# Optimization experiments

Measured on AMD Instinct MI355X. Metric: run time of the kernel, lower is better.

## Reference

```python
import jax, jax.numpy as jnp
import numpy as np

B, T, IN = 32, 1024, 256
H = 128          # hidden_size
NL = 2           # num_layers
NC = 4           # num_classes
F2 = 2 * H       # bidirectional feature size


def _lstm_dir(xs, w_ih, w_hh, b_ih, b_hh, reverse):
    # xs: [T, B, in]; w_ih: [4H, in]; w_hh: [4H, H]
    if reverse:
        xs = xs[::-1]
    h0 = jnp.zeros((xs.shape[1], H), xs.dtype)
    c0 = jnp.zeros((xs.shape[1], H), xs.dtype)

    def step(carry, xt):
        h, c = carry
        g = xt @ w_ih.T + b_ih + h @ w_hh.T + b_hh  # [B, 4H]
        i, f, gg, o = jnp.split(g, 4, axis=-1)       # PyTorch gate order i,f,g,o
        c = jax.nn.sigmoid(f) * c + jax.nn.sigmoid(i) * jnp.tanh(gg)
        h = jax.nn.sigmoid(o) * jnp.tanh(c)
        return (h, c), h

    _, hs = jax.lax.scan(step, (h0, c0), xs)  # [T, B, H]
    if reverse:
        hs = hs[::-1]
    return hs


def setup_inputs() -> dict:
    key = jax.random.key(0)
    ks = jax.random.split(key, 12)
    s = 0.05
    x = jax.random.normal(ks[0], (B, T, IN), jnp.float32)
    # stacked LSTM params: [layer, direction, ...]; layer0 in = IN, layer1 in = 2H = IN
    w_ih = jax.random.normal(ks[1], (NL, 2, 4 * H, IN), jnp.float32) * s
    w_hh = jax.random.normal(ks[2], (NL, 2, 4 * H, H), jnp.float32) * s
    b_ih = jax.random.normal(ks[3], (NL, 2, 4 * H), jnp.float32) * s
    b_hh = jax.random.normal(ks[4], (NL, 2, 4 * H), jnp.float32) * s
    wq = jax.random.normal(ks[5], (F2, F2), jnp.float32) * s
    wk = jax.random.normal(ks[6], (F2, F2), jnp.float32) * s
    wv = jax.random.normal(ks[7], (F2, F2), jnp.float32) * s
    bq = jax.random.normal(ks[8], (F2,), jnp.float32) * s
    bk = jax.random.normal(ks[9], (F2,), jnp.float32) * s
    bv = jax.random.normal(ks[10], (F2,), jnp.float32) * s
    w_fc = jax.random.normal(ks[11], (NC, F2), jnp.float32) * s
    b_fc = jnp.zeros((NC,), jnp.float32)
    return {"x": x, "w_ih": w_ih, "w_hh": w_hh, "b_ih": b_ih, "b_hh": b_hh,
            "wq": wq, "wk": wk, "wv": wv, "bq": bq, "bk": bk, "bv": bv,
            "w_fc": w_fc, "b_fc": b_fc}


def reference(x, w_ih, w_hh, b_ih, b_hh, wq, wk, wv, bq, bk, bv, w_fc, b_fc):
    # --- biLSTM (eval mode: inter-layer dropout inactive) ---
    xs = jnp.swapaxes(x, 0, 1)  # time-major [T, B, IN]
    for l in range(NL):
        fwd = _lstm_dir(xs, w_ih[l, 0], w_hh[l, 0], b_ih[l, 0], b_hh[l, 0], False)
        bwd = _lstm_dir(xs, w_ih[l, 1], w_hh[l, 1], b_ih[l, 1], b_hh[l, 1], True)
        xs = jnp.concatenate([fwd, bwd], axis=-1)  # [T, B, 2H]
    out = jnp.swapaxes(xs, 0, 1)  # [B, T, 2H]
    # --- naive full self-attention ---
    q = out @ wq.T + bq
    k = out @ wk.T + bk
    v = out @ wv.T + bv
    scores = jnp.einsum('btd,bsd->bts', q, k) / jnp.sqrt(jnp.float32(F2))
    attn = jax.nn.softmax(scores, axis=-1)          # [B, T, T]
    ctx = jnp.einsum('bts,bsd->btd', attn, v)       # [B, T, 2H]
    # --- FC head on last timestep ---
    return ctx[:, -1, :] @ w_fc.T + b_fc            # [B, NC]
```

## Files before the change

### kernel.cpp

```cpp
#include <hip/hip_runtime.h>
#include <math.h>
#include <stdint.h>

#define BB 32
#define TT 1024
#define HH 128
#define G4 512
#define CH 16
#define XPS 516

typedef _Float16 half2_t __attribute__((ext_vector_type(2)));
typedef _Float16 half8_t __attribute__((ext_vector_type(8)));
typedef float f32x4 __attribute__((ext_vector_type(4)));

__device__ __forceinline__ float fdot2f(half2_t a, half2_t b, float c) {
    return __builtin_amdgcn_fdot2(a, b, c, false);
}
__device__ __forceinline__ float rcpf(float x) {
    return __builtin_amdgcn_rcpf(x);
}
__device__ __forceinline__ float dpp_xor1(float x) {
    return __builtin_bit_cast(float, __builtin_amdgcn_update_dpp(
        0, __builtin_bit_cast(int, x), 0xB1, 0xF, 0xF, true));
}
__device__ __forceinline__ float dpp_xor2(float x) {
    return __builtin_bit_cast(float, __builtin_amdgcn_update_dpp(
        0, __builtin_bit_cast(int, x), 0x4E, 0xF, 0xF, true));
}
__device__ __forceinline__ void bar_lgkm() {
    asm volatile("s_waitcnt lgkmcnt(0)\n\ts_barrier" ::: "memory");
}

__global__ __launch_bounds__(256) void cvt_wih(
    const float* __restrict__ w, _Float16* __restrict__ o)
{
    const int i = (blockIdx.x * 256 + threadIdx.x) * 4;
    float4 f = *(const float4*)(w + i);
    half2_t t[2] = { half2_t{(_Float16)f.x, (_Float16)f.y},
                     half2_t{(_Float16)f.z, (_Float16)f.w} };
    *(float2*)(o + i) = *(float2*)t;
}

__global__ __launch_bounds__(512, 1) void lstm_fused(
    const float* __restrict__ x_in,
    const _Float16* __restrict__ wih16_l,
    const float* __restrict__ b_ih_l,
    const float* __restrict__ b_hh_l,
    const float* __restrict__ w_hh_l,
    float* __restrict__ out)
{
    const int b = blockIdx.x & 31;
    const int d = blockIdx.x >> 5;
    const int tid = threadIdx.x;
    const int wvid = tid >> 6;
    const int l = tid & 63;
    const int s = l & 3;
    const int g = l >> 2;
    const int j = (wvid << 4) | g;

    __shared__ __align__(16) _Float16 hs[HH];
    __shared__ __align__(16) float xp[2][CH * XPS];
    __shared__ __align__(16) half2_t xr[2][CH * 128];
    __shared__ __align__(16) float obuf[CH * HH];

    half2_t wv[4][16];
#pragma unroll
    for (int G = 0; G < 4; ++G) {
        const float* wr = w_hh_l + (size_t)(d * G4 + 128 * G + j) * HH + 32 * s;
#pragma unroll
        for (int q4 = 0; q4 < 8; ++q4) {
            float4 f = *(const float4*)(wr + 4 * q4);
            wv[G][2 * q4]     = half2_t{(_Float16)f.x, (_Float16)f.y};
            wv[G][2 * q4 + 1] = half2_t{(_Float16)f.z, (_Float16)f.w};
        }
    }

    const int acol0 = wvid * 64 + (l & 15);
    const _Float16* wn = wih16_l + ((size_t)d * G4 + acol0) * 256 + (l >> 4) * 8;
    const float bias0 = b_ih_l[d * G4 + acol0]      + b_hh_l[d * G4 + acol0];
    const float bias1 = b_ih_l[d * G4 + acol0 + 16] + b_hh_l[d * G4 + acol0 + 16];
    const float bias2 = b_ih_l[d * G4 + acol0 + 32] + b_hh_l[d * G4 + acol0 + 32];
    const float bias3 = b_ih_l[d * G4 + acol0 + 48] + b_hh_l[d * G4 + acol0 + 48];

    const int cbase = ((acol0 & 127) << 2) + (acol0 >> 7);

    const float* xbase = x_in + (size_t)b * TT * 256;

    const int a_noswz = (l & 15) * 512 + (l >> 4) * 16;
    const int a_swz   = (l & 7) << 4;
    const int w_swz_byte = (tid * 16) ^ (((tid >> 5) & 7) << 4);

#pragma unroll 1
    for (int p = 0; p < 2; ++p) {
        const int tlo = d ? (1008 - p * CH) : p * CH;
        const float* gs = xbase + (size_t)tlo * 256 + tid * 8;
        float4 f0 = *(const float4*)gs;
        float4 f1 = *(const float4*)(gs + 4);
        half2_t t4[4] = { half2_t{(_Float16)f0.x, (_Float16)f0.y},
                          half2_t{(_Float16)f0.z, (_Float16)f0.w},
                          half2_t{(_Float16)f1.x, (_Float16)f1.y},
                          half2_t{(_Float16)f1.z, (_Float16)f1.w} };
        *(float4*)((char*)xr[p] + w_swz_byte) = *(float4*)t4;
    }
    __syncthreads();

    f32x4 acc0 = {bias0, bias0, bias0, bias0};
    f32x4 acc1 = {bias1, bias1, bias1, bias1};
    f32x4 acc2 = {bias2, bias2, bias2, bias2};
    f32x4 acc3 = {bias3, bias3, bias3, bias3};

#pragma unroll
    for (int kt = 0; kt < 8; ++kt) {
        half8_t af = *(const half8_t*)((const char*)xr[0] + ((a_noswz + kt * 64) ^ a_swz));
        acc0 = __builtin_amdgcn_mfma_f32_16x16x32_f16(af, *(const half8_t*)(wn +         kt * 32), acc0, 0, 0, 0);
        acc1 = __builtin_amdgcn_mfma_f32_16x16x32_f16(af, *(const half8_t*)(wn +  4096 + kt * 32), acc1, 0, 0, 0);
        acc2 = __builtin_amdgcn_mfma_f32_16x16x32_f16(af, *(const half8_t*)(wn +  8192 + kt * 32), acc2, 0, 0, 0);
        acc3 = __builtin_amdgcn_mfma_f32_16x16x32_f16(af, *(const half8_t*)(wn + 12288 + kt * 32), acc3, 0, 0, 0);
    }
    {
        const int rb = (l >> 4) * 4;
#pragma unroll
        for (int q = 0; q < 4; ++q) {
            const int ix = (rb + q) * XPS + cbase;
            xp[0][ix]       = acc0[q];
            xp[0][ix + 64]  = acc1[q];
            xp[0][ix + 128] = acc2[q];
            xp[0][ix + 192] = acc3[q];
        }
    }
    acc0 = (f32x4){bias0, bias0, bias0, bias0};
    acc1 = (f32x4){bias1, bias1, bias1, bias1};
    acc2 = (f32x4){bias2, bias2, bias2, bias2};
    acc3 = (f32x4){bias3, bias3, bias3, bias3};

    if (tid < 64) ((half2_t*)hs)[tid] = half2_t{(_Float16)0.f, (_Float16)0.f};
    float c = 0.f;
    float* ob = out + (size_t)b * TT * 256 + d * HH;
    __syncthreads();

    float4 rg0 = {}, rg1 = {};
    for (int ck = 0; ck < 64; ++ck) {
        const int cur = ck & 1;
        const bool doproj = (ck + 1 < 64);
        if (ck + 2 < 64) {
            const int tlo2 = d ? (1008 - (ck + 2) * CH) : (ck + 2) * CH;
            const float* gs = xbase + (size_t)tlo2 * 256 + tid * 8;
            rg0 = *(const float4*)gs;
            rg1 = *(const float4*)(gs + 4);
        }
        const float* xb = xp[cur];
        const char* xr_rd = (const char*)xr[cur ^ 1];

        auto rec_step = [&](int si) {
            const int lds_t = d ? (CH - 1 - si) : si;
            const float4 xg4 = *(const float4*)&xb[lds_t * XPS + (j << 2)];

            const float4* hp = (const float4*)(hs + 32 * s);
            float4 hA = hp[0], hB = hp[1], hC = hp[2], hD = hp[3];
            half2_t hh[16];
            hh[0]  = __builtin_bit_cast(half2_t, hA.x);
            hh[1]  = __builtin_bit_cast(half2_t, hA.y);
            hh[2]  = __builtin_bit_cast(half2_t, hA.z);
            hh[3]  = __builtin_bit_cast(half2_t, hA.w);
            hh[4]  = __builtin_bit_cast(half2_t, hB.x);
            hh[5]  = __builtin_bit_cast(half2_t, hB.y);
            hh[6]  = __builtin_bit_cast(half2_t, hB.z);
            hh[7]  = __builtin_bit_cast(half2_t, hB.w);
            hh[8]  = __builtin_bit_cast(half2_t, hC.x);
            hh[9]  = __builtin_bit_cast(half2_t, hC.y);
            hh[10] = __builtin_bit_cast(half2_t, hC.z);
            hh[11] = __builtin_bit_cast(half2_t, hC.w);
            hh[12] = __builtin_bit_cast(half2_t, hD.x);
            hh[13] = __builtin_bit_cast(half2_t, hD.y);
            hh[14] = __builtin_bit_cast(half2_t, hD.z);
            hh[15] = __builtin_bit_cast(half2_t, hD.w);

            float a0 = 0.f, a1 = 0.f, a2 = 0.f, a3 = 0.f;
            float e0 = 0.f, e1 = 0.f, e2 = 0.f, e3 = 0.f;
#pragma unroll
            for (int kk = 0; kk < 8; ++kk) {
                a0 = fdot2f(wv[0][kk], hh[kk], a0);
                a1 = fdot2f(wv[1][kk], hh[kk], a1);
                a2 = fdot2f(wv[2][kk], hh[kk], a2);
                a3 = fdot2f(wv[3][kk], hh[kk], a3);
                e0 = fdot2f(wv[0][kk + 8], hh[kk + 8], e0);
                e1 = fdot2f(wv[1][kk + 8], hh[kk + 8], e1);
                e2 = fdot2f(wv[2][kk + 8], hh[kk + 8], e2);
                e3 = fdot2f(wv[3][kk + 8], hh[kk + 8], e3);
            }
            a0 += e0; a1 += e1; a2 += e2; a3 += e3;

            a0 += dpp_xor1(a0); a0 += dpp_xor2(a0);
            a1 += dpp_xor1(a1); a1 += dpp_xor2(a1);
            a2 += dpp_xor1(a2); a2 += dpp_xor2(a2);
            a3 += dpp_xor1(a3); a3 += dpp_xor2(a3);

            const float gi = rcpf(1.f + __expf(-(a0 + xg4.x)));
            const float gf = rcpf(1.f + __expf(-(a1 + xg4.y)));
            const float gg = 1.f - 2.f * rcpf(1.f + __expf(2.f * (a2 + xg4.z)));
            const float go = rcpf(1.f + __expf(-(a3 + xg4.w)));
            c = gf * c + gi * gg;
            const float th = 1.f - 2.f * rcpf(1.f + __expf(2.f * c));
            const float h = go * th;
            if (s == 0) {
                hs[j] = (_Float16)h;
                obuf[si * HH + j] = h;
            }
        };

        half8_t gbEA = {}, gbEB = {}, gbOA = {}, gbOB = {};
        if (doproj) {
            gbEA = *(const half8_t*)(wn);
            gbEB = *(const half8_t*)(wn + 4096);
        }

#pragma unroll 1
        for (int sp = 0; sp < CH / 2; ++sp) {
            const int kt = sp;
            half8_t afrag = {};
            if (doproj) {
                afrag = *(const half8_t*)(xr_rd + ((a_noswz + kt * 64) ^ a_swz));
                gbOA = *(const half8_t*)(wn +  8192 + kt * 32);
                gbOB = *(const half8_t*)(wn + 12288 + kt * 32);
            }
            rec_step(2 * sp);
            if (doproj) {
                acc0 = __builtin_amdgcn_mfma_f32_16x16x32_f16(afrag, gbEA, acc0, 0, 0, 0);
                acc1 = __builtin_amdgcn_mfma_f32_16x16x32_f16(afrag, gbEB, acc1, 0, 0, 0);
            }
            bar_lgkm();
            if (doproj) {
                const int ktn = (kt + 1) & 7;
                gbEA = *(const half8_t*)(wn +        ktn * 32);
                gbEB = *(const half8_t*)(wn + 4096 + ktn * 32);
            }
            rec_step(2 * sp + 1);
            if (doproj) {
                acc2 = __builtin_amdgcn_mfma_f32_16x16x32_f16(afrag, gbOA, acc2, 0, 0, 0);
                acc3 = __builtin_amdgcn_mfma_f32_16x16x32_f16(afrag, gbOB, acc3, 0, 0, 0);
            }
            bar_lgkm();
        }

        {
            const int idx = tid * 4;
            const int sf = idx >> 7, jf = idx & 127;
            const int sg = ck * CH + sf;
            const int t  = d ? (TT - 1 - sg) : sg;
            float4 o0 = *(const float4*)&obuf[idx];
            *(float4*)&ob[(size_t)t * 256 + jf] = o0;
        }
        if (doproj) {
            float* xpn = xp[cur ^ 1];
            const int rb = (l >> 4) * 4;
#pragma unroll
            for (int q = 0; q < 4; ++q) {
                const int ix = (rb + q) * XPS + cbase;
                xpn[ix]       = acc0[q];
                xpn[ix + 64]  = acc1[q];
                xpn[ix + 128] = acc2[q];
                xpn[ix + 192] = acc3[q];
            }
            acc0 = (f32x4){bias0, bias0, bias0, bias0};
            acc1 = (f32x4){bias1, bias1, bias1, bias1};
            acc2 = (f32x4){bias2, bias2, bias2, bias2};
            acc3 = (f32x4){bias3, bias3, bias3, bias3};
        }
        if (ck + 2 < 64) {
            half2_t t4[4] = { half2_t{(_Float16)rg0.x, (_Float16)rg0.y},
                              half2_t{(_Float16)rg0.z, (_Float16)rg0.w},
                              half2_t{(_Float16)rg1.x, (_Float16)rg1.y},
                              half2_t{(_Float16)rg1.z, (_Float16)rg1.w} };
            *(float4*)((char*)xr[cur] + w_swz_byte) = *(float4*)t4;
        }
        __syncthreads();
    }
}

__global__ __launch_bounds__(1024) void attn_kernel(
    const float* __restrict__ out1,
    const float* __restrict__ wq, const float* __restrict__ bq,
    const float* __restrict__ wk,
    const float* __restrict__ wv, const float* __restrict__ bv,
    const float* __restrict__ wfc, const float* __restrict__ bfc,
    float* __restrict__ outp)
{
    const int b = blockIdx.x;
    const int tid = threadIdx.x;
    const int n = tid & 255, qq = tid >> 8;

    __shared__ float xl[256], q[256], u[256], cx[256];
    __shared__ __align__(16) float r[256];
    __shared__ float sc[TT];
    __shared__ float red[1024];
    __shared__ float part[4][256];

    const float* ob = out1 + (size_t)b * TT * 256;

    if (tid < 256) xl[tid] = ob[(size_t)(TT - 1) * 256 + tid];
    __syncthreads();

    {
        float a = 0.f;
        const float* wr = wq + (size_t)n * 256 + qq * 64;
        const float* xq = xl + qq * 64;
#pragma unroll 8
        for (int k = 0; k < 64; ++k) a += xq[k] * wr[k];
        part[qq][n] = a;
    }
    __syncthreads();
    if (tid < 256) q[tid] = bq[tid] + part[0][tid] + part[1][tid] + part[2][tid] + part[3][tid];
    __syncthreads();

    {
        float a = 0.f;
        const float* wkp = wk + (size_t)(qq * 64) * 256 + n;
#pragma unroll 8
        for (int dd = 0; dd < 64; ++dd) a += q[qq * 64 + dd] * wkp[(size_t)dd * 256];
        part[qq][n] = a;
    }
    __syncthreads();
    if (tid < 256) r[tid] = part[0][tid] + part[1][tid] + part[2][tid] + part[3][tid];
    __syncthreads();

    {
        const int wave = tid >> 6, lane = tid & 63;
        float4 r4 = *(const float4*)&r[lane * 4];
        for (int t = wave; t < TT; t += 16) {
            float4 o4 = *(const float4*)(ob + (size_t)t * 256 + lane * 4);
            float p = r4.x * o4.x + r4.y * o4.y + r4.z * o4.z + r4.w * o4.w;
#pragma unroll
            for (int off = 32; off > 0; off >>= 1) p += __shfl_down(p, off, 64);
            if (lane == 0) sc[t] = p * 0.0625f;
        }
    }
    __syncthreads();

    float v = sc[tid];
    red[tid] = v; __syncthreads();
    for (int st = 512; st > 0; st >>= 1) {
        if (tid < st) red[tid] = fmaxf(red[tid], red[tid + st]);
        __syncthreads();
    }
    const float mx = red[0]; __syncthreads();
    const float e = expf(v - mx);
    sc[tid] = e;
    red[tid] = e; __syncthreads();
    for (int st = 512; st > 0; st >>= 1) {
        if (tid < st) red[tid] += red[tid + st];
        __syncthreads();
    }
    const float inv = 1.f / red[0];
    __syncthreads();

    {
        float a = 0.f;
        const float* op = ob + (size_t)(qq * 256) * 256 + n;
        const float* sp = sc + qq * 256;
#pragma unroll 4
        for (int t = 0; t < 256; ++t) a += sp[t] * op[(size_t)t * 256];
        part[qq][n] = a;
    }
    __syncthreads();
    if (tid < 256) u[tid] = (part[0][tid] + part[1][tid] + part[2][tid] + part[3][tid]) * inv;
    __syncthreads();

    {
        float a = 0.f;
        const float* wr = wv + (size_t)n * 256 + qq * 64;
#pragma unroll 8
        for (int k = 0; k < 64; ++k) a += u[qq * 64 + k] * wr[k];
        part[qq][n] = a;
    }
    __syncthreads();
    if (tid < 256) cx[tid] = bv[tid] + part[0][tid] + part[1][tid] + part[2][tid] + part[3][tid];
    __syncthreads();

    if (tid < 4) {
        float o = bfc[tid];
        for (int k = 0; k < 256; ++k) o += cx[k] * wfc[tid * 256 + k];
        outp[b * 4 + tid] = o;
    }
}

extern "C" void kernel_launch(void* const* d_in, const int* in_sizes, int n_in,
                              void* d_out, int out_size, void* d_ws, size_t ws_size,
                              hipStream_t stream)
{
    const float* x    = (const float*)d_in[0];
    const float* w_ih = (const float*)d_in[1];
    const float* w_hh = (const float*)d_in[2];
    const float* b_ih = (const float*)d_in[3];
    const float* b_hh = (const float*)d_in[4];
    const float* wq   = (const float*)d_in[5];
    const float* wk   = (const float*)d_in[6];
    const float* wv   = (const float*)d_in[7];
    const float* bq   = (const float*)d_in[8];
    const float* bv   = (const float*)d_in[10];
    const float* wfc  = (const float*)d_in[11];
    const float* bfcv = (const float*)d_in[12];
    float* outp = (float*)d_out;

    float* ws = (float*)d_ws;
    _Float16* wih16 = (_Float16*)ws;
    float* out0 = ws + 262144;
    float* out1 = out0 + 8388608;

    cvt_wih<<<512, 256, 0, stream>>>(w_ih, wih16);

    lstm_fused<<<64, 512, 0, stream>>>(x, wih16, b_ih, b_hh, w_hh, out0);
    lstm_fused<<<64, 512, 0, stream>>>(out0, wih16 + 262144, b_ih + 1024, b_hh + 1024,
                                       w_hh + 2 * 512 * 128, out1);
    attn_kernel<<<32, 1024, 0, stream>>>(out1, wq, bq, wk, wv, bv, wfc, bfcv, outp);
}
```

Before: 1.688 ms.

## Keep input-projection weights in registers and stage x prefetch via global_load_lds

Preloads all W_ih fp16 fragments for the input projection into registers once, instead of reloading them from global memory on every chunk. The next chunk of x is now copied by async global-to-LDS loads into a staging buffer, then converted to fp16 after a vmcnt wait, rather than held in registers across the chunk. The inner step loop is fully unrolled. This adds heavy register pressure (128 extra VGPRs on top of the W_hh fragments), which risks spills or lower occupancy. The staged data is read by different threads than the ones that loaded it, and only a per-thread vmcnt wait guards that read.

```diff
diff --git a/kernel.cpp b/kernel.cpp
--- a/kernel.cpp
+++ b/kernel.cpp
@@ -12,6 +12,8 @@
 typedef _Float16 half2_t __attribute__((ext_vector_type(2)));
 typedef _Float16 half8_t __attribute__((ext_vector_type(8)));
 typedef float f32x4 __attribute__((ext_vector_type(4)));
+typedef __attribute__((address_space(3))) uint32_t lds_u32;
+typedef __attribute__((address_space(1))) const uint32_t glb_u32;
 
 __device__ __forceinline__ float fdot2f(half2_t a, half2_t b, float c) {
     return __builtin_amdgcn_fdot2(a, b, c, false);
@@ -62,6 +64,7 @@
     __shared__ __align__(16) float xp[2][CH * XPS];
     __shared__ __align__(16) half2_t xr[2][CH * 128];
     __shared__ __align__(16) float obuf[CH * HH];
+    __shared__ __align__(16) float xstage[CH * 256];
 
     half2_t wv[4][16];
 #pragma unroll
@@ -81,6 +84,15 @@
     const float bias1 = b_ih_l[d * G4 + acol0 + 16] + b_hh_l[d * G4 + acol0 + 16];
     const float bias2 = b_ih_l[d * G4 + acol0 + 32] + b_hh_l[d * G4 + acol0 + 32];
     const float bias3 = b_ih_l[d * G4 + acol0 + 48] + b_hh_l[d * G4 + acol0 + 48];
+
+    half8_t wf0[8], wf1[8], wf2[8], wf3[8];
+#pragma unroll
+    for (int kt = 0; kt < 8; ++kt) {
+        wf0[kt] = *(const half8_t*)(wn +         kt * 32);
+        wf1[kt] = *(const half8_t*)(wn +  4096 + kt * 32);
+        wf2[kt] = *(const half8_t*)(wn +  8192 + kt * 32);
+        wf3[kt] = *(const half8_t*)(wn + 12288 + kt * 32);
+    }
 
     const int cbase = ((acol0 & 127) << 2) + (acol0 >> 7);
 
@@ -112,10 +124,10 @@
 #pragma unroll
     for (int kt = 0; kt < 8; ++kt) {
         half8_t af = *(const half8_t*)((const char*)xr[0] + ((a_noswz + kt * 64) ^ a_swz));
-        acc0 = __builtin_amdgcn_mfma_f32_16x16x32_f16(af, *(const half8_t*)(wn +         kt * 32), acc0, 0, 0, 0);
-        acc1 = __builtin_amdgcn_mfma_f32_16x16x32_f16(af, *(const half8_t*)(wn +  4096 + kt * 32), acc1, 0, 0, 0);
-        acc2 = __builtin_amdgcn_mfma_f32_16x16x32_f16(af, *(const half8_t*)(wn +  8192 + kt * 32), acc2, 0, 0, 0);
-        acc3 = __builtin_amdgcn_mfma_f32_16x16x32_f16(af, *(const half8_t*)(wn + 12288 + kt * 32), acc3, 0, 0, 0);
+        acc0 = __builtin_amdgcn_mfma_f32_16x16x32_f16(af, wf0[kt], acc0, 0, 0, 0);
+        acc1 = __builtin_amdgcn_mfma_f32_16x16x32_f16(af, wf1[kt], acc1, 0, 0, 0);
+        acc2 = __builtin_amdgcn_mfma_f32_16x16x32_f16(af, wf2[kt], acc2, 0, 0, 0);
+        acc3 = __builtin_amdgcn_mfma_f32_16x16x32_f16(af, wf3[kt], acc3, 0, 0, 0);
     }
     {
         const int rb = (l >> 4) * 4;
@@ -138,15 +150,18 @@
     float* ob = out + (size_t)b * TT * 256 + d * HH;
     __syncthreads();
 
-    float4 rg0 = {}, rg1 = {};
     for (int ck = 0; ck < 64; ++ck) {
         const int cur = ck & 1;
         const bool doproj = (ck + 1 < 64);
         if (ck + 2 < 64) {
             const int tlo2 = d ? (1008 - (ck + 2) * CH) : (ck + 2) * CH;
-            const float* gs = xbase + (size_t)tlo2 * 256 + tid * 8;
-            rg0 = *(const float4*)gs;
-            rg1 = *(const float4*)(gs + 4);
+            const float* gsrc = xbase + (size_t)tlo2 * 256;
+#pragma unroll
+            for (int cc = 0; cc < 2; ++cc)
+                __builtin_amdgcn_global_load_lds(
+                    (glb_u32*)(gsrc + tid * 4 + cc * 2048),
+                    (lds_u32*)&xstage[tid * 4 + cc * 2048],
+                    16, 0, 0);
         }
         const float* xb = xp[cur];
         const char* xr_rd = (const char*)xr[cur ^ 1];
@@ -208,36 +223,21 @@
             }
         };
 
-        half8_t gbEA = {}, gbEB = {}, gbOA = {}, gbOB = {};
-        if (doproj) {
-            gbEA = *(const half8_t*)(wn);
-            gbEB = *(const half8_t*)(wn + 4096);
-        }
-
-#pragma unroll 1
+#pragma unroll
         for (int sp = 0; sp < CH / 2; ++sp) {
-            const int kt = sp;
             half8_t afrag = {};
-            if (doproj) {
-                afrag = *(const half8_t*)(xr_rd + ((a_noswz + kt * 64) ^ a_swz));
-                gbOA = *(const half8_t*)(wn +  8192 + kt * 32);
-                gbOB = *(const half8_t*)(wn + 12288 + kt * 32);
-            }
+            if (doproj)
+                afrag = *(const half8_t*)(xr_rd + ((a_noswz + sp * 64) ^ a_swz));
             rec_step(2 * sp);
             if (doproj) {
-                acc0 = __builtin_amdgcn_mfma_f32_16x16x32_f16(afrag, gbEA, acc0, 0, 0, 0);
-                acc1 = __builtin_amdgcn_mfma_f32_16x16x32_f16(afrag, gbEB, acc1, 0, 0, 0);
+                acc0 = __builtin_amdgcn_mfma_f32_16x16x32_f16(afrag, wf0[sp], acc0, 0, 0, 0);
+                acc1 = __builtin_amdgcn_mfma_f32_16x16x32_f16(afrag, wf1[sp], acc1, 0, 0, 0);
             }
             bar_lgkm();
-            if (doproj) {
-                const int ktn = (kt + 1) & 7;
-                gbEA = *(const half8_t*)(wn +        ktn * 32);
-                gbEB = *(const half8_t*)(wn + 4096 + ktn * 32);
-            }
             rec_step(2 * sp + 1);
             if (doproj) {
-                acc2 = __builtin_amdgcn_mfma_f32_16x16x32_f16(afrag, gbOA, acc2, 0, 0, 0);
-                acc3 = __builtin_amdgcn_mfma_f32_16x16x32_f16(afrag, gbOB, acc3, 0, 0, 0);
+                acc2 = __builtin_amdgcn_mfma_f32_16x16x32_f16(afrag, wf2[sp], acc2, 0, 0, 0);
+                acc3 = __builtin_amdgcn_mfma_f32_16x16x32_f16(afrag, wf3[sp], acc3, 0, 0, 0);
             }
             bar_lgkm();
         }
@@ -267,10 +267,13 @@
             acc3 = (f32x4){bias3, bias3, bias3, bias3};
         }
         if (ck + 2 < 64) {
-            half2_t t4[4] = { half2_t{(_Float16)rg0.x, (_Float16)rg0.y},
-                              half2_t{(_Float16)rg0.z, (_Float16)rg0.w},
-                              half2_t{(_Float16)rg1.x, (_Float16)rg1.y},
-                              half2_t{(_Float16)rg1.z, (_Float16)rg1.w} };
+            asm volatile("s_waitcnt vmcnt(0)" ::: "memory");
+            float4 f0 = *(const float4*)&xstage[tid * 8];
+            float4 f1 = *(const float4*)&xstage[tid * 8 + 4];
+            half2_t t4[4] = { half2_t{(_Float16)f0.x, (_Float16)f0.y},
+                              half2_t{(_Float16)f0.z, (_Float16)f0.w},
+                              half2_t{(_Float16)f1.x, (_Float16)f1.y},
+                              half2_t{(_Float16)f1.z, (_Float16)f1.w} };
             *(float4*)((char*)xr[cur] + w_swz_byte) = *(float4*)t4;
         }
         __syncthreads();
```

Result: slower. 1.767 ms (+4.7%).

## Split attention head into three kernels spreading time chunks across more blocks

Applied to the files above, without the earlier changes.

Replaces the single 32-block attention kernel with three kernels: one that computes the query-key projection vector per batch, one with 256 blocks that each score 128 timesteps and accumulate an unnormalised context and softmax denominator through global atomics, and a final kernel that normalises, applies the value projection and the FC head. This spreads the bandwidth-heavy pass over out1 across many more CUs. The max subtraction is dropped from the softmax, which risks overflow for large scores, and float atomics make summation order nondeterministic. Two extra launches are added.

```diff
diff --git a/kernel.cpp b/kernel.cpp
--- a/kernel.cpp
+++ b/kernel.cpp
@@ -277,103 +277,93 @@
     }
 }
 
-__global__ __launch_bounds__(1024) void attn_kernel(
-    const float* __restrict__ out1,
-    const float* __restrict__ wq, const float* __restrict__ bq,
-    const float* __restrict__ wk,
-    const float* __restrict__ wv, const float* __restrict__ bv,
-    const float* __restrict__ wfc, const float* __restrict__ bfc,
-    float* __restrict__ outp)
+
+__global__ __launch_bounds__(256) void attn_qr(
+    const float* __restrict__ out1, const float* __restrict__ wq,
+    const float* __restrict__ bq,   const float* __restrict__ wk,
+    float* __restrict__ r_ws, float* __restrict__ ctxw, float* __restrict__ den)
 {
     const int b = blockIdx.x;
     const int tid = threadIdx.x;
-    const int n = tid & 255, qq = tid >> 8;
-
-    __shared__ float xl[256], q[256], u[256], cx[256];
+    __shared__ float xl[256], q[256];
+    const float* ob = out1 + (size_t)b * TT * 256;
+
+    xl[tid] = ob[(size_t)(TT - 1) * 256 + tid];
+    ctxw[b * 256 + tid] = 0.f;
+    if (tid == 0) den[b] = 0.f;
+    __syncthreads();
+
+    float acc = bq[tid];
+    const float* wqr = wq + (size_t)tid * 256;
+#pragma unroll 4
+    for (int k = 0; k < 256; ++k) acc += xl[k] * wqr[k];
+    q[tid] = acc;
+    __syncthreads();
+
+    acc = 0.f;
+#pragma unroll 4
+    for (int dd = 0; dd < 256; ++dd) acc += q[dd] * wk[(size_t)dd * 256 + tid];
+    r_ws[b * 256 + tid] = acc * 0.0625f;
+}
+
+__global__ __launch_bounds__(256) void attn_sc(
+    const float* __restrict__ out1, const float* __restrict__ r_ws,
+    float* __restrict__ ctxw, float* __restrict__ den)
+{
+    const int b  = blockIdx.x >> 3;
+    const int s8 = blockIdx.x & 7;
+    const int tid = threadIdx.x;
     __shared__ __align__(16) float r[256];
-    __shared__ float sc[TT];
-    __shared__ float red[1024];
-    __shared__ float part[4][256];
-
-    const float* ob = out1 + (size_t)b * TT * 256;
-
-    if (tid < 256) xl[tid] = ob[(size_t)(TT - 1) * 256 + tid];
-    __syncthreads();
-
-    {
-        float a = 0.f;
-        const float* wr = wq + (size_t)n * 256 + qq * 64;
-        const float* xq = xl + qq * 64;
-#pragma unroll 8
-        for (int k = 0; k < 64; ++k) a += xq[k] * wr[k];
-        part[qq][n] = a;
-    }
-    __syncthreads();
-    if (tid < 256) q[tid] = bq[tid] + part[0][tid] + part[1][tid] + part[2][tid] + part[3][tid];
-    __syncthreads();
-
-    {
-        float a = 0.f;
-        const float* wkp = wk + (size_t)(qq * 64) * 256 + n;
-#pragma unroll 8
-        for (int dd = 0; dd < 64; ++dd) a += q[qq * 64 + dd] * wkp[(size_t)dd * 256];
-        part[qq][n] = a;
-    }
-    __syncthreads();
-    if (tid < 256) r[tid] = part[0][tid] + part[1][tid] + part[2][tid] + part[3][tid];
-    __syncthreads();
-
-    {
-        const int wave = tid >> 6, lane = tid & 63;
-        float4 r4 = *(const float4*)&r[lane * 4];
-        for (int t = wave; t < TT; t += 16) {
-            float4 o4 = *(const float4*)(ob + (size_t)t * 256 + lane * 4);
-            float p = r4.x * o4.x + r4.y * o4.y + r4.z * o4.z + r4.w * o4.w;
-#pragma unroll
-            for (int off = 32; off > 0; off >>= 1) p += __shfl_down(p, off, 64);
-            if (lane == 0) sc[t] = p * 0.0625f;
-        }
-    }
-    __syncthreads();
-
-    float v = sc[tid];
-    red[tid] = v; __syncthreads();
-    for (int st = 512; st > 0; st >>= 1) {
-        if (tid < st) red[tid] = fmaxf(red[tid], red[tid + st]);
-        __syncthreads();
-    }
-    const float mx = red[0]; __syncthreads();
-    const float e = expf(v - mx);
-    sc[tid] = e;
-    red[tid] = e; __syncthreads();
-    for (int st = 512; st > 0; st >>= 1) {
+    __shared__ float ev[128];
+    __shared__ float red[256];
+
+    const float* ob = out1 + (size_t)b * TT * 256 + (size_t)s8 * 128 * 256;
+    r[tid] = r_ws[b * 256 + tid];
+    __syncthreads();
+
+    const int wave = tid >> 6, lane = tid & 63;
+    float4 r4 = *(const float4*)&r[lane * 4];
+    for (int t = wave; t < 128; t += 4) {
+        float4 o4 = *(const float4*)(ob + (size_t)t * 256 + lane * 4);
+        float p = r4.x * o4.x + r4.y * o4.y + r4.z * o4.z + r4.w * o4.w;
+#pragma unroll
+        for (int off = 32; off > 0; off >>= 1) p += __shfl_down(p, off, 64);
+        if (lane == 0) ev[t] = expf(p);
+    }
+    __syncthreads();
+
+    red[tid] = (tid < 128) ? ev[tid] : 0.f;
+    __syncthreads();
+    for (int st = 128; st > 0; st >>= 1) {
         if (tid < st) red[tid] += red[tid + st];
         __syncthreads();
     }
-    const float inv = 1.f / red[0];
-    __syncthreads();
-
-    {
-        float a = 0.f;
-        const float* op = ob + (size_t)(qq * 256) * 256 + n;
-        const float* sp = sc + qq * 256;
+    if (tid == 0) atomicAdd(&den[b], red[0]);
+
+    float a = 0.f;
 #pragma unroll 4
-        for (int t = 0; t < 256; ++t) a += sp[t] * op[(size_t)t * 256];
-        part[qq][n] = a;
-    }
-    __syncthreads();
-    if (tid < 256) u[tid] = (part[0][tid] + part[1][tid] + part[2][tid] + part[3][tid]) * inv;
-    __syncthreads();
-
-    {
-        float a = 0.f;
-        const float* wr = wv + (size_t)n * 256 + qq * 64;
-#pragma unroll 8
-        for (int k = 0; k < 64; ++k) a += u[qq * 64 + k] * wr[k];
-        part[qq][n] = a;
-    }
-    __syncthreads();
-    if (tid < 256) cx[tid] = bv[tid] + part[0][tid] + part[1][tid] + part[2][tid] + part[3][tid];
+    for (int t = 0; t < 128; ++t) a += ev[t] * ob[(size_t)t * 256 + tid];
+    atomicAdd(&ctxw[b * 256 + tid], a);
+}
+
+__global__ __launch_bounds__(256) void attn_fc(
+    const float* __restrict__ ctxw, const float* __restrict__ den,
+    const float* __restrict__ wv,   const float* __restrict__ bv,
+    const float* __restrict__ wfc,  const float* __restrict__ bfc,
+    float* __restrict__ outp)
+{
+    const int b = blockIdx.x;
+    const int tid = threadIdx.x;
+    __shared__ float u[256], cx[256];
+
+    u[tid] = ctxw[b * 256 + tid] / den[b];
+    __syncthreads();
+
+    float acc = bv[tid];
+    const float* wr = wv + (size_t)tid * 256;
+#pragma unroll 4
+    for (int k = 0; k < 256; ++k) acc += u[k] * wr[k];
+    cx[tid] = acc;
     __syncthreads();
 
     if (tid < 4) {
@@ -405,11 +395,17 @@
     _Float16* wih16 = (_Float16*)ws;
     float* out0 = ws + 262144;
     float* out1 = out0 + 8388608;
+    float* r_ws = out1 + 8388608;
+    float* ctxw = r_ws + 8192;
+    float* den  = ctxw + 8192;
 
     cvt_wih<<<512, 256, 0, stream>>>(w_ih, wih16);
 
     lstm_fused<<<64, 512, 0, stream>>>(x, wih16, b_ih, b_hh, w_hh, out0);
     lstm_fused<<<64, 512, 0, stream>>>(out0, wih16 + 262144, b_ih + 1024, b_hh + 1024,
                                        w_hh + 2 * 512 * 128, out1);
-    attn_kernel<<<32, 1024, 0, stream>>>(out1, wq, bq, wk, wv, bv, wfc, bfcv, outp);
-}
+
+    attn_qr<<<32, 256, 0, stream>>>(out1, wq, bq, wk, r_ws, ctxw, den);
+    attn_sc<<<256, 256, 0, stream>>>(out1, r_ws, ctxw, den);
+    attn_fc<<<32, 256, 0, stream>>>(ctxw, den, wv, bv, wfc, bfcv, outp);
+}
```

Result: no change. 1.679 ms (-0.5%).
